# Optimization experiments

Hardware: AMD Instinct MI355X
Metric: run time of the kernel (lower is better)

Reference implementation:

```python
import jax, jax.numpy as jnp
import numpy as np

B, T, C = 4, 2048, 1024
H = 16
HD = C // H


def setup_inputs() -> dict:
    key = jax.random.key(0)
    k1, k2, k3 = jax.random.split(key, 3)
    x = jax.random.normal(k1, (B, T, C), dtype=jnp.float32)
    w_qkv = jax.random.normal(k2, (C, 3 * C), dtype=jnp.float32) * (C ** -0.5)
    w_proj = jax.random.normal(k3, (C, C), dtype=jnp.float32) * (C ** -0.5)
    b_proj = jnp.zeros((C,), dtype=jnp.float32)
    return {"x": x, "w_qkv": w_qkv, "w_proj": w_proj, "b_proj": b_proj}


def reference(x, w_qkv, w_proj, b_proj):
    Bd, Td, Cd = x.shape
    scale = HD ** -0.5
    qkv = x @ w_qkv  # [B,T,3C]
    q, k, v = jnp.split(qkv, 3, axis=-1)
    # [B,H,T,HD]
    q = q.reshape(Bd, Td, H, HD).transpose(0, 2, 1, 3)
    k = k.reshape(Bd, Td, H, HD).transpose(0, 2, 1, 3)
    v = v.reshape(Bd, Td, H, HD).transpose(0, 2, 1, 3)
    att = jnp.einsum('bhqd,bhkd->bhqk', q, k) * scale
    causal = jnp.triu(jnp.ones((Td, Td), dtype=bool), k=1)
    att = jnp.where(causal, -jnp.inf, att)
    att = jax.nn.softmax(att, axis=-1)
    y = jnp.einsum('bhqk,bhkd->bhqd', att, v)
    y = y.transpose(0, 2, 1, 3).reshape(Bd, Td, Cd)
    return y @ w_proj + b_proj
```

## Files before the change

kernel.cpp:

```cpp
#include <hip/hip_runtime.h>

typedef unsigned short u16;
typedef __attribute__((ext_vector_type(8))) short short8;
typedef __attribute__((ext_vector_type(4))) short short4v;
typedef __attribute__((ext_vector_type(4))) float floatx4;
typedef __attribute__((ext_vector_type(4))) unsigned short ushort4v;

#define B_ 4
#define T_ 2048
#define C_ 1024
#define H_ 16
#define HD_ 64

template <bool V> struct BC { static constexpr bool value = V; };
template <int N> struct ICN { static constexpr int v = N; };

static __device__ __forceinline__ u16 f2bf(float f) {
  union { float f; unsigned int i; } c; c.f = f;
  unsigned int u = c.i;
  return (u16)((u + 0x7FFFu + ((u >> 16) & 1u)) >> 16);
}
static __device__ __forceinline__ unsigned pk2(float lo, float hi) {
  union { float f; unsigned u; } a, b; a.f = hi; b.f = lo;
  return __builtin_amdgcn_perm(a.u, b.u, 0x07060302u);
}
static __device__ __forceinline__ unsigned pk2r(float lo, float hi) {
  return (unsigned)f2bf(lo) | ((unsigned)f2bf(hi) << 16);
}

static __device__ __forceinline__ void gload16(const u16* g, u16* l) {
  __builtin_amdgcn_global_load_lds(
      (const __attribute__((address_space(1))) unsigned int*)(g),
      (__attribute__((address_space(3))) unsigned int*)(l), 16, 0, 0);
}

template <int N> static __device__ __forceinline__ void wait_vm_bar() {
  if constexpr (N == 6)
    asm volatile("s_waitcnt vmcnt(6)\n\ts_barrier" ::: "memory");
  else if constexpr (N == 4)
    asm volatile("s_waitcnt vmcnt(4)\n\ts_barrier" ::: "memory");
  else if constexpr (N == 0)
    asm volatile("s_waitcnt vmcnt(0)\n\ts_barrier" ::: "memory");
}

__global__ __launch_bounds__(256) void prep_k(const float* __restrict__ x,
                                              const float* __restrict__ w_qkv,
                                              const float* __restrict__ w_proj,
                                              u16* __restrict__ xbf,
                                              u16* __restrict__ wqkvT,
                                              u16* __restrict__ wprojT) {
  const int bid = blockIdx.x;
  if (bid < 8192) {
    const int i = bid * 256 + threadIdx.x;
    const float4 f = ((const float4*)x)[i];
    ushort4v o;
    o.x = f2bf(f.x); o.y = f2bf(f.y); o.z = f2bf(f.z); o.w = f2bf(f.w);
    *(ushort4v*)(xbf + (size_t)i * 4) = o;
    return;
  }
  __shared__ u16 tile[32][33];
  const float* in;
  u16* out;
  int R, Cc, tb;
  if (bid < 11264) {
    in = w_qkv; out = wqkvT; R = C_; Cc = 3 * C_; tb = bid - 8192;
  } else {
    in = w_proj; out = wprojT; R = C_; Cc = C_; tb = bid - 11264;
  }
  const int tpr = Cc / 32;
  const int bx = (tb % tpr) * 32;
  const int by = (tb / tpr) * 32;
  const int tx = threadIdx.x & 31;
  const int ty = threadIdx.x >> 5;
  #pragma unroll
  for (int i = ty; i < 32; i += 8)
    tile[i][tx] = f2bf(in[(size_t)(by + i) * Cc + bx + tx]);
  __syncthreads();
  #pragma unroll
  for (int i = ty; i < 32; i += 8)
    out[(size_t)(bx + i) * R + by + tx] = tile[tx][i];
}

template <int MODE, int NFR>
__global__ __launch_bounds__(256, 2) void gemm4w(const u16* __restrict__ A,
                                                 const u16* __restrict__ Bt,
                                                 u16* __restrict__ outb,
                                                 u16* __restrict__ outv,
                                                 float* __restrict__ outf,
                                                 const float* __restrict__ bias,
                                                 int M, int N) {
  constexpr int TN = NFR * 32;
  constexpr int BUFA = 4096;
  constexpr int BUFB = TN * 32;
  constexpr int BUF = BUFA + BUFB;
  constexpr int LPW = (8 + TN / 16) / 4;
  __shared__ __align__(16) u16 lds[3 * BUF];

  const int bid = blockIdx.x;
  const int xcd = bid & 7;
  const int loc = bid >> 3;
  const int tM = (xcd * 8 + (loc & 7)) * 128;
  const int tN = (loc >> 3) * TN;
  const int tid = threadIdx.x;
  const int wave = tid >> 6;
  const int lane = tid & 63;
  const int lr = lane & 15;
  const int quad = lane >> 4;
  const int wm = wave >> 1;
  const int wn = wave & 1;
  const int csw = (lr >> 1) & 3;
  const int srow = lane >> 2;
  const int skofs = ((lane & 3) ^ ((lane >> 3) & 3)) * 8;

  const u16* gbase[LPW];
  int ldst[LPW];
  #pragma unroll
  for (int j = 0; j < LPW; j++) {
    const int s = wave * LPW + j;
    if (s < 8) {
      gbase[j] = A + (size_t)(tM + s * 16 + srow) * 1024 + skofs;
      ldst[j] = s * 512;
    } else {
      gbase[j] = Bt + (size_t)(tN + (s - 8) * 16 + srow) * 1024 + skofs;
      ldst[j] = BUFA + (s - 8) * 512;
    }
  }

  const floatx4 zf = {0.f, 0.f, 0.f, 0.f};
  floatx4 acc[4][NFR];
  #pragma unroll
  for (int i = 0; i < 4; i++)
    #pragma unroll
    for (int j = 0; j < NFR; j++) acc[i][j] = zf;

  auto stage = [&](int t, int buf) {
    #pragma unroll
    for (int j = 0; j < LPW; j++)
      gload16(gbase[j] + t * 32, &lds[buf * BUF + ldst[j]]);
  };

  auto ktile = [&](int t, int buf, auto VM) {
    constexpr int vm = decltype(VM)::v;
    const u16* lA = &lds[buf * BUF];
    const u16* lB = lA + BUFA;
    short8 af[4], bfr[NFR];
    #pragma unroll
    for (int mt = 0; mt < 4; mt++)
      af[mt] = *(const short8*)(&lA[(wm * 64 + mt * 16 + lr) * 32 + ((quad ^ csw) * 8)]);
    #pragma unroll
    for (int nt = 0; nt < NFR; nt++)
      bfr[nt] = *(const short8*)(&lB[(wn * (NFR * 16) + nt * 16 + lr) * 32 + ((quad ^ csw) * 8)]);
    if constexpr (vm > 0) stage(t + 2, (buf + 2) % 3);
    __builtin_amdgcn_s_setprio(1);
    #pragma unroll
    for (int mt = 0; mt < 4; mt++)
      #pragma unroll
      for (int nt = 0; nt < NFR; nt++)
        acc[mt][nt] = __builtin_amdgcn_mfma_f32_16x16x32_bf16(af[mt], bfr[nt],
                                                              acc[mt][nt], 0, 0, 0);
    __builtin_amdgcn_s_setprio(0);
    if constexpr (vm > 0) wait_vm_bar<LPW>();
    else if constexpr (vm == 0) wait_vm_bar<0>();
  };

  stage(0, 0); stage(1, 1);
  wait_vm_bar<LPW>();

  for (int tb = 0; tb < 10; ++tb) {
    const int t = tb * 3;
    ktile(t,     0, ICN<LPW>{});
    ktile(t + 1, 1, ICN<LPW>{});
    ktile(t + 2, 2, ICN<LPW>{});
  }
  ktile(30, 0, ICN<0>{});
  ktile(31, 1, ICN<-1>{});

  if constexpr (MODE == 1) {
    if (tN >= 2 * C_) {
      asm volatile("s_barrier" ::: "memory");
      #pragma unroll
      for (int mt = 0; mt < 4; mt++) {
        const int t0 = wm * 64 + mt * 16 + quad * 4;
        #pragma unroll
        for (int nt = 0; nt < NFR; nt++) {
          const int vrow = wn * (NFR * 16) + nt * 16 + lr;
          u16* p = &lds[vrow * 128 + (((t0 >> 3) ^ (vrow & 7)) * 8) + (t0 & 7)];
          *(unsigned*)(p)     = pk2r(acc[mt][nt][0], acc[mt][nt][1]);
          *(unsigned*)(p + 2) = pk2r(acc[mt][nt][2], acc[mt][nt][3]);
        }
      }
      asm volatile("s_waitcnt lgkmcnt(0)\n\ts_barrier" ::: "memory");
      const int b = tM >> 11;
      const int t0b = tM & (T_ - 1);
      const int h0 = (tN - 2 * C_) >> 6;
      u16* vb = outv + (size_t)(b * H_ + h0) * HD_ * T_;
      #pragma unroll
      for (int i = 0; i < 16; i++) {
        const int lin = tid + i * 256;
        const int row = lin >> 4;
        const int chv = lin & 15;
        const short8 v = *(const short8*)(&lds[row * 128 + ((chv ^ (row & 7)) * 8)]);
        *(short8*)(vb + (size_t)row * T_ + t0b + chv * 8) = v;
      }
      return;
    }
    #pragma unroll
    for (int mt = 0; mt < 4; mt++) {
      const int m0 = tM + wm * 64 + mt * 16 + quad * 4;
      #pragma unroll
      for (int nt = 0; nt < NFR; nt++) {
        const int n = tN + wn * (NFR * 16) + nt * 16 + lr;
        #pragma unroll
        for (int r = 0; r < 4; r++)
          outb[(size_t)(m0 + r) * N + n] = f2bf(acc[mt][nt][r]);
      }
    }
  } else {
    #pragma unroll
    for (int mt = 0; mt < 4; mt++) {
      const int m0 = tM + wm * 64 + mt * 16 + quad * 4;
      #pragma unroll
      for (int nt = 0; nt < NFR; nt++) {
        const int n = tN + wn * (NFR * 16) + nt * 16 + lr;
        const float bv = bias[n];
        #pragma unroll
        for (int r = 0; r < 4; r++)
          __builtin_nontemporal_store(acc[mt][nt][r] + bv,
                                      &outf[(size_t)(m0 + r) * N + n]);
      }
    }
  }
}

__global__ __launch_bounds__(256, 4) void attn_k(const u16* __restrict__ qkv,
                                                 const u16* __restrict__ vt,
                                                 u16* __restrict__ y) {
  __shared__ __align__(16) u16 Ks[2 * 4096];
  __shared__ __align__(16) u16 Vs[2 * 4096];
  const int bid = blockIdx.x;
  const int s = bid >> 3;
  const int qp = s >> 3;
  const int bh = ((s & 7) << 3) | (bid & 7);
  const int b = bh >> 4, h = bh & 15;
  const int tid = threadIdx.x;
  const int wave = tid >> 6;
  const int lane = tid & 63;
  const int lr = lane & 15;
  const int quad = lane >> 4;
  const int qtA = qp, qtB = 31 - qp;

  const int srow = lane >> 3;
  const int skofs = ((lane & 7) ^ ((lane >> 3) & 7)) * 8;
  const int gsw = lr & 7;

  const size_t RS = 3 * C_;
  const u16* qcol = qkv + (size_t)b * T_ * RS + h * HD_;
  const u16* kcol = qcol + C_;

  const size_t qrA = (size_t)(qtA * 64 + wave * 16 + lr) * RS;
  const size_t qrB = (size_t)(qtB * 64 + wave * 16 + lr) * RS;
  const short8 aq0A = *(const short8*)(qcol + qrA + quad * 8);
  const short8 aq1A = *(const short8*)(qcol + qrA + 32 + quad * 8);
  const short8 aq0B = *(const short8*)(qcol + qrB + quad * 8);
  const short8 aq1B = *(const short8*)(qcol + qrB + 32 + quad * 8);

  const floatx4 zf = {0.f, 0.f, 0.f, 0.f};
  const float C1 = 0.125f * 1.44269504f;
  const float C2 = -16.0f * 1.44269504f;
  const short8 vones = {16256, 16256, 16256, 16256, 16256, 16256, 16256, 16256};

  floatx4 accA[4], accB[4];
  floatx4 accSA = zf, accSB = zf;
  #pragma unroll
  for (int i = 0; i < 4; i++) { accA[i] = zf; accB[i] = zf; }

  auto stage = [&](int kt, int buf) {
    #pragma unroll
    for (int j = 0; j < 2; j++) {
      const int seg = wave * 2 + j;
      const int row = seg * 8 + srow;
      gload16(kcol + (size_t)(kt * 64 + row) * RS + skofs, &Ks[buf * 4096 + seg * 512]);
      gload16(vt + ((size_t)bh * HD_ + row) * T_ + kt * 64 + skofs, &Vs[buf * 4096 + seg * 512]);
    }
    __builtin_amdgcn_sched_barrier(0);
  };

  auto core = [&](int cur, auto WA, auto DA, auto DB) {
    constexpr bool wA = decltype(WA)::value;
    constexpr bool dA = decltype(DA)::value;
    constexpr bool dB = decltype(DB)::value;
    const u16* Kb = &Ks[cur * 4096];
    const u16* Vb = &Vs[cur * 4096];
    float peA[4][4], peB[4][4];
    #pragma unroll
    for (int nt = 0; nt < 4; nt++) {
      const short8 bk0 =
          *(const short8*)(&Kb[(nt * 16 + lr) * 64 + ((quad ^ gsw) * 8)]);
      const short8 bk1 =
          *(const short8*)(&Kb[(nt * 16 + lr) * 64 + (((quad + 4) ^ gsw) * 8)]);
      {
        floatx4 st = __builtin_amdgcn_mfma_f32_16x16x32_bf16(
            bk1, aq1B,
            __builtin_amdgcn_mfma_f32_16x16x32_bf16(bk0, aq0B, zf, 0, 0, 0),
            0, 0, 0);
        #pragma unroll
        for (int r = 0; r < 4; r++) {
          float pe = __builtin_amdgcn_exp2f(fmaf(st[r], C1, C2));
          if constexpr (dB)
            if (nt * 16 + quad * 4 + r > wave * 16 + lr) pe = 0.f;
          peB[nt][r] = pe;
        }
      }
      if constexpr (wA) {
        floatx4 st = __builtin_amdgcn_mfma_f32_16x16x32_bf16(
            bk1, aq1A,
            __builtin_amdgcn_mfma_f32_16x16x32_bf16(bk0, aq0A, zf, 0, 0, 0),
            0, 0, 0);
        #pragma unroll
        for (int r = 0; r < 4; r++) {
          float pe = __builtin_amdgcn_exp2f(fmaf(st[r], C1, C2));
          if constexpr (dA)
            if (nt * 16 + quad * 4 + r > wave * 16 + lr) pe = 0.f;
          peA[nt][r] = pe;
        }
      }
    }

    short8 pB[2], pA[2];
    #pragma unroll
    for (int h2 = 0; h2 < 2; h2++) {
      union { unsigned u[4]; short8 s8; } w;
      w.u[0] = pk2(peB[2 * h2][0], peB[2 * h2][1]);
      w.u[1] = pk2(peB[2 * h2][2], peB[2 * h2][3]);
      w.u[2] = pk2(peB[2 * h2 + 1][0], peB[2 * h2 + 1][1]);
      w.u[3] = pk2(peB[2 * h2 + 1][2], peB[2 * h2 + 1][3]);
      pB[h2] = w.s8;
    }
    if constexpr (wA) {
      #pragma unroll
      for (int h2 = 0; h2 < 2; h2++) {
        union { unsigned u[4]; short8 s8; } w;
        w.u[0] = pk2(peA[2 * h2][0], peA[2 * h2][1]);
        w.u[1] = pk2(peA[2 * h2][2], peA[2 * h2][3]);
        w.u[2] = pk2(peA[2 * h2 + 1][0], peA[2 * h2 + 1][1]);
        w.u[3] = pk2(peA[2 * h2 + 1][2], peA[2 * h2 + 1][3]);
        pA[h2] = w.s8;
      }
    }

    #pragma unroll
    for (int h2 = 0; h2 < 2; h2++) {
      accSB = __builtin_amdgcn_mfma_f32_16x16x32_bf16(vones, pB[h2], accSB, 0, 0, 0);
      if constexpr (wA)
        accSA = __builtin_amdgcn_mfma_f32_16x16x32_bf16(vones, pA[h2], accSA, 0, 0, 0);
      #pragma unroll
      for (int dt = 0; dt < 4; dt++) {
        const int base = (dt * 16 + lr) * 64;
        const int cl = h2 * 4 + (quad >> 1);
        const int off_lo = ((cl ^ gsw) * 8) + (quad & 1) * 4;
        const int off_hi = (((cl + 2) ^ gsw) * 8) + (quad & 1) * 4;
        const short4v vlo = *(const short4v*)(&Vb[base + off_lo]);
        const short4v vhi = *(const short4v*)(&Vb[base + off_hi]);
        const short8 av = __builtin_shufflevector(vlo, vhi, 0, 1, 2, 3, 4, 5, 6, 7);
        accB[dt] = __builtin_amdgcn_mfma_f32_16x16x32_bf16(av, pB[h2], accB[dt], 0, 0, 0);
        if constexpr (wA)
          accA[dt] = __builtin_amdgcn_mfma_f32_16x16x32_bf16(av, pA[h2], accA[dt], 0, 0, 0);
      }
    }
  };

  stage(0, 0);
  asm volatile("s_waitcnt vmcnt(0)\n\ts_barrier" ::: "memory");
  int cur = 0;
  for (int kt = 0; kt < qtA; kt++) {
    stage(kt + 1, cur ^ 1);
    core(cur, BC<true>{}, BC<false>{}, BC<false>{});
    asm volatile("s_waitcnt vmcnt(0)\n\ts_barrier" ::: "memory");
    cur ^= 1;
  }
  stage(qtA + 1, cur ^ 1);
  core(cur, BC<true>{}, BC<true>{}, BC<false>{});
  asm volatile("s_waitcnt vmcnt(0)\n\ts_barrier" ::: "memory");
  cur ^= 1;
  for (int kt = qtA + 1; kt < qtB; kt++) {
    stage(kt + 1, cur ^ 1);
    core(cur, BC<false>{}, BC<false>{}, BC<false>{});
    asm volatile("s_waitcnt vmcnt(0)\n\ts_barrier" ::: "memory");
    cur ^= 1;
  }
  core(cur, BC<false>{}, BC<false>{}, BC<true>{});

  #pragma unroll
  for (int ph = 0; ph < 2; ph++) {
    const int qt = ph ? qtB : qtA;
    const floatx4* acc = ph ? accB : accA;
    const float inv = 1.f / (ph ? accSB[0] : accSA[0]);
    const int qg = qt * 64 + wave * 16 + lr;
    u16* yrow = y + ((size_t)(b * T_ + qg)) * C_ + h * HD_;
    #pragma unroll
    for (int dt = 0; dt < 4; dt++) {
      ushort4v o;
      #pragma unroll
      for (int r = 0; r < 4; r++) o[r] = f2bf(acc[dt][r] * inv);
      *(ushort4v*)(yrow + dt * 16 + quad * 4) = o;
    }
  }
}

extern "C" void kernel_launch(void* const* d_in, const int* in_sizes, int n_in,
                              void* d_out, int out_size, void* d_ws, size_t ws_size,
                              hipStream_t stream) {
  const float* x      = (const float*)d_in[0];
  const float* w_qkv  = (const float*)d_in[1];
  const float* w_proj = (const float*)d_in[2];
  const float* b_proj = (const float*)d_in[3];
  float* out = (float*)d_out;

  u16* ws = (u16*)d_ws;
  const size_t SZ = (size_t)B_ * T_ * C_;
  u16* xbf    = ws;
  u16* wqkvT  = xbf + SZ;
  u16* wprojT = wqkvT + (size_t)3 * C_ * C_;
  u16* qkvw   = wprojT + (size_t)C_ * C_;
  u16* vtw    = qkvw + 3 * SZ;
  u16* yw     = xbf;

  prep_k<<<12288, 256, 0, stream>>>(x, w_qkv, w_proj, xbf, wqkvT, wprojT);
  gemm4w<1, 8><<<768, 256, 0, stream>>>(
      xbf, wqkvT, qkvw, vtw, nullptr, nullptr, B_ * T_, 3 * C_);
  attn_k<<<1024, 256, 0, stream>>>(qkvw, vtw, yw);
  gemm4w<2, 4><<<512, 256, 0, stream>>>(
      yw, wprojT, nullptr, nullptr, out, b_proj, B_ * T_, C_);
}
```

Measured before the change: 231.9 us.

## Pre-permute V^T columns in QKV epilogue and fold softmax scale into Q

The QKV GEMM epilogue now writes V^T with its key columns permuted so the attention kernel can fetch each V operand with a single 16-byte LDS read instead of two 8-byte reads plus a shuffle. Q is also pre-multiplied by scale*log2(e) before bf16 rounding, which removes the per-element FMA ahead of exp2 in the attention inner loop. The fixed -16 max offset is dropped, so exp2 now runs on unshifted logits; this risks overflow or precision changes if scores get large, and Q's bf16 rounding now happens after scaling.

```diff
diff --git a/kernel.cpp b/kernel.cpp
--- a/kernel.cpp
+++ b/kernel.cpp
@@ -198,12 +198,22 @@
       for (int i = 0; i < 16; i++) {
         const int lin = tid + i * 256;
         const int row = lin >> 4;
-        const int chv = lin & 15;
-        const short8 v = *(const short8*)(&lds[row * 128 + ((chv ^ (row & 7)) * 8)]);
-        *(short8*)(vb + (size_t)row * T_ + t0b + chv * 8) = v;
+        const int cp = lin & 15;
+        const int g = cp >> 3;
+        const int cc = cp & 7;
+        const int ct0 = g * 8 + ((cc >> 2) & 1) * 4 + ((cc >> 1) & 1);
+        const int o4 = (cc & 1) * 4;
+        const int rs = row & 7;
+        const short4v s0 =
+            *(const short4v*)(&lds[row * 128 + ((ct0 ^ rs) * 8) + o4]);
+        const short4v s1 =
+            *(const short4v*)(&lds[row * 128 + (((ct0 + 2) ^ rs) * 8) + o4]);
+        const short8 v = __builtin_shufflevector(s0, s1, 0, 1, 2, 3, 4, 5, 6, 7);
+        *(short8*)(vb + (size_t)row * T_ + t0b + cp * 8) = v;
       }
       return;
     }
+    const float qs = (tN < C_) ? 0.18033688f : 1.0f;
     #pragma unroll
     for (int mt = 0; mt < 4; mt++) {
       const int m0 = tM + wm * 64 + mt * 16 + quad * 4;
@@ -212,7 +222,7 @@
         const int n = tN + wn * (NFR * 16) + nt * 16 + lr;
         #pragma unroll
         for (int r = 0; r < 4; r++)
-          outb[(size_t)(m0 + r) * N + n] = f2bf(acc[mt][nt][r]);
+          outb[(size_t)(m0 + r) * N + n] = f2bf(acc[mt][nt][r] * qs);
       }
     }
   } else {
@@ -265,8 +275,6 @@
   const short8 aq1B = *(const short8*)(qcol + qrB + 32 + quad * 8);
 
   const floatx4 zf = {0.f, 0.f, 0.f, 0.f};
-  const float C1 = 0.125f * 1.44269504f;
-  const float C2 = -16.0f * 1.44269504f;
   const short8 vones = {16256, 16256, 16256, 16256, 16256, 16256, 16256, 16256};
 
   floatx4 accA[4], accB[4];
@@ -305,7 +313,7 @@
             0, 0, 0);
         #pragma unroll
         for (int r = 0; r < 4; r++) {
-          float pe = __builtin_amdgcn_exp2f(fmaf(st[r], C1, C2));
+          float pe = __builtin_amdgcn_exp2f(st[r]);
           if constexpr (dB)
             if (nt * 16 + quad * 4 + r > wave * 16 + lr) pe = 0.f;
           peB[nt][r] = pe;
@@ -318,7 +326,7 @@
             0, 0, 0);
         #pragma unroll
         for (int r = 0; r < 4; r++) {
-          float pe = __builtin_amdgcn_exp2f(fmaf(st[r], C1, C2));
+          float pe = __builtin_amdgcn_exp2f(st[r]);
           if constexpr (dA)
             if (nt * 16 + quad * 4 + r > wave * 16 + lr) pe = 0.f;
           peA[nt][r] = pe;
@@ -355,13 +363,8 @@
         accSA = __builtin_amdgcn_mfma_f32_16x16x32_bf16(vones, pA[h2], accSA, 0, 0, 0);
       #pragma unroll
       for (int dt = 0; dt < 4; dt++) {
-        const int base = (dt * 16 + lr) * 64;
-        const int cl = h2 * 4 + (quad >> 1);
-        const int off_lo = ((cl ^ gsw) * 8) + (quad & 1) * 4;
-        const int off_hi = (((cl + 2) ^ gsw) * 8) + (quad & 1) * 4;
-        const short4v vlo = *(const short4v*)(&Vb[base + off_lo]);
-        const short4v vhi = *(const short4v*)(&Vb[base + off_hi]);
-        const short8 av = __builtin_shufflevector(vlo, vhi, 0, 1, 2, 3, 4, 5, 6, 7);
+        const short8 av = *(const short8*)(
+            &Vb[(dt * 16 + lr) * 64 + (((h2 * 4 + quad) ^ gsw) * 8)]);
         accB[dt] = __builtin_amdgcn_mfma_f32_16x16x32_bf16(av, pB[h2], accB[dt], 0, 0, 0);
         if constexpr (wA)
           accA[dt] = __builtin_amdgcn_mfma_f32_16x16x32_bf16(av, pA[h2], accA[dt], 0, 0, 0);
```

Measured after the change: 223.6 us. 3.6% less time.
